# Performance work log

Measured on AMD Instinct MI355X. Metric: run time of the kernel, lower is better.

The kernel has to match this reference:

```python
import jax, jax.numpy as jnp
from jax import lax
import numpy as np

S = 0.025
EPS = 1e-6


def setup_inputs() -> dict:
    key = jax.random.key(0)
    k1, = jax.random.split(key, 1)
    B, F, T = 64, 128, 4000
    x = jax.random.uniform(k1, (B, F, T), dtype=jnp.float32)  # nonnegative spectrogram
    log_gain = jnp.zeros((F,), dtype=jnp.float32)
    log_bias = jnp.zeros((F,), dtype=jnp.float32)
    log_power = jnp.zeros((F,), dtype=jnp.float32)
    return {"x": x, "log_gain": log_gain, "log_bias": log_bias, "log_power": log_power}


def _ema(x):
    # x: [B, F, T]; first-order IIR m_t = (1-s)*m_{t-1} + s*x_t, m_{-1} = x_0
    # (so m_0 = x_0, matching the torch loop's init last_state = x[:, :, 0]).
    xt = jnp.moveaxis(x, -1, 0)  # [T, B, F]

    def step(carry, x_t):
        m = (1.0 - S) * carry + S * x_t
        return m, m

    _, m = lax.scan(step, xt[0], xt)
    return jnp.moveaxis(m, 0, -1)  # [B, F, T]


def reference(x, log_gain, log_bias, log_power):
    m = _ema(x)
    g = jnp.exp(log_gain)[None, :, None]   # [1, F, 1]
    b = jnp.exp(log_bias)[None, :, None]
    p = jnp.exp(log_power)[None, :, None]
    return (x / (m + EPS) ** g + b) ** p - b ** p
```

## Files before the change

kernel.cpp:

```cpp
#include <hip/hip_runtime.h>


#define LOG2F(v) __builtin_amdgcn_logf(v)
#define EXP2F(v) __builtin_amdgcn_exp2f(v)

constexpr int   T_LEN = 4000;
constexpr int   F_DIM = 128;
constexpr int   EPT   = 16;
constexpr int   TPB   = 256;
constexpr int   ACTIVE = T_LEN / EPT;
constexpr float S_C   = 0.025f;
constexpr float A1    = 1.0f - S_C;
constexpr float EPS_C = 1e-6f;

constexpr float pow_n(double a, int n) {
    double r = 1.0;
    for (int i = 0; i < n; ++i) r *= a;
    return (float)r;
}
constexpr float A16 = pow_n((double)A1, EPT);

__global__ __launch_bounds__(TPB) void pcen_kernel(
    const float* __restrict__ x,
    const float* __restrict__ log_gain,
    const float* __restrict__ log_bias,
    const float* __restrict__ log_power,
    float* __restrict__ out)
{
    const int row  = blockIdx.x;
    const int f    = row & (F_DIM - 1);
    const long long base = (long long)row * T_LEN;
    const int tid  = threadIdx.x;
    const int lane = tid & 63;
    const int wid  = tid >> 6;
    const bool active = tid < ACTIVE;

    const float g  = expf(log_gain[f]);
    const float b  = expf(log_bias[f]);
    const float p  = expf(log_power[f]);
    const float bp = EXP2F(p * LOG2F(b));

    float xv[EPT];
    const float4* xin = reinterpret_cast<const float4*>(x + base) + tid * 4;
    if (active) {
        #pragma unroll
        for (int q = 0; q < 4; ++q) {
            float4 v = xin[q];
            xv[q*4 + 0] = v.x; xv[q*4 + 1] = v.y;
            xv[q*4 + 2] = v.z; xv[q*4 + 3] = v.w;
        }
    }

    float Bi = 0.0f;
    if (active) {
        #pragma unroll
        for (int j = 0; j < EPT; ++j) Bi = fmaf(A1, Bi, S_C * xv[j]);
    }
    float Ai = active ? A16 : 1.0f;

    #pragma unroll
    for (int d = 1; d < 64; d <<= 1) {
        float Ap = __shfl_up(Ai, d);
        float Bp = __shfl_up(Bi, d);
        if (lane >= d) { Bi = fmaf(Ai, Bp, Bi); Ai *= Ap; }
    }

    __shared__ float sA[4], sB[4], sM0;
    if (lane == 63) { sA[wid] = Ai; sB[wid] = Bi; }
    if (tid == 0)   { sM0 = xv[0]; }
    __syncthreads();

    float pA = 1.0f, pB = 0.0f;
    for (int w = 0; w < wid; ++w) { pB = fmaf(sA[w], pB, sB[w]); pA *= sA[w]; }

    float eA = __shfl_up(Ai, 1);
    float eB = __shfl_up(Bi, 1);
    if (lane == 0) { eA = 1.0f; eB = 0.0f; }

    float m = fmaf(eA, fmaf(pA, sM0, pB), eB);

    if (active) {
        float4* o4 = reinterpret_cast<float4*>(out + base) + tid * 4;
        #pragma unroll
        for (int q = 0; q < 4; ++q) {
            float4 o;
            float ov[4];
            #pragma unroll
            for (int j = 0; j < 4; ++j) {
                const float xj = xv[q*4 + j];
                m = fmaf(A1, m, S_C * xj);
                float v = xj * EXP2F(-g * LOG2F(m + EPS_C));
                ov[j] = EXP2F(p * LOG2F(v + b)) - bp;
            }
            o.x = ov[0]; o.y = ov[1]; o.z = ov[2]; o.w = ov[3];
            o4[q] = o;
        }
    }
}

extern "C" void kernel_launch(void* const* d_in, const int* in_sizes, int n_in,
                              void* d_out, int out_size, void* d_ws, size_t ws_size,
                              hipStream_t stream) {
    const float* x  = (const float*)d_in[0];
    const float* lg = (const float*)d_in[1];
    const float* lb = (const float*)d_in[2];
    const float* lp = (const float*)d_in[3];
    float* out = (float*)d_out;

    const int rows = in_sizes[0] / T_LEN;
    pcen_kernel<<<dim3(rows), dim3(TPB), 0, stream>>>(x, lg, lb, lp, out);
}
```

Before: 238.4 us.

## Process one row per wavefront in LDS-transposed chunks with parameter fast path

Restructures the kernel so each wavefront owns a whole row, streaming it in four 1024-element chunks that are double-buffered in registers and transposed through padded LDS so each lane scans 16 consecutive samples. The cross-block scan becomes a wave-only shuffle scan with constant decay powers, and the carry between chunks comes from a lane-63 broadcast. A runtime fast path is added for gain, bias and power all exactly one, replacing the log/exp chain with a reciprocal. This removes the block-wide sync and most transcendentals on the test inputs, at the cost of more LDS traffic and a serial dependency across chunks.

```diff
diff --git a/kernel.cpp b/kernel.cpp
--- a/kernel.cpp
+++ b/kernel.cpp
@@ -1,24 +1,105 @@
 #include <hip/hip_runtime.h>
 
 
+#define EXP2F(v) __builtin_amdgcn_exp2f(v)
 #define LOG2F(v) __builtin_amdgcn_logf(v)
-#define EXP2F(v) __builtin_amdgcn_exp2f(v)
+#define RCPF(v)  __builtin_amdgcn_rcpf(v)
 
 constexpr int   T_LEN = 4000;
 constexpr int   F_DIM = 128;
-constexpr int   EPT   = 16;
 constexpr int   TPB   = 256;
-constexpr int   ACTIVE = T_LEN / EPT;
+constexpr int   RPB   = 4;
 constexpr float S_C   = 0.025f;
-constexpr float A1    = 1.0f - S_C;
+constexpr float A1    = 0.975f;
 constexpr float EPS_C = 1e-6f;
+constexpr int   LROW  = 17;
+constexpr int   WSLICE = 64 * LROW;
 
-constexpr float pow_n(double a, int n) {
-    double r = 1.0;
-    for (int i = 0; i < n; ++i) r *= a;
-    return (float)r;
+constexpr double dpow(double a, int n){ double r = 1; for (int i = 0; i < n; ++i) r *= a; return r; }
+constexpr float K1  = (float)dpow(0.975, 16);
+constexpr float K2  = (float)dpow(0.975, 32);
+constexpr float K4  = (float)dpow(0.975, 64);
+constexpr float K8  = (float)dpow(0.975, 128);
+constexpr float K16 = (float)dpow(0.975, 256);
+constexpr float K32 = (float)dpow(0.975, 512);
+constexpr float C16 = -0.5844128f;
+
+struct RowParams { float g, b, p, bp; bool fast; };
+
+template<int NF4>
+__device__ __forceinline__ void load_chunk(const float4* xr4, int c, int lane, float4 B[4]) {
+    #pragma unroll
+    for (int r = 0; r < 4; ++r) {
+        const int i4 = r * 64 + lane;
+        if (NF4 == 256 || i4 < NF4) B[r] = xr4[c * 256 + i4];
+        else                        B[r] = make_float4(0.f, 0.f, 0.f, 0.f);
+    }
 }
-constexpr float A16 = pow_n((double)A1, EPT);
+
+__device__ __forceinline__ void stage_chunk(float* L, int tw, const float4 B[4]) {
+    #pragma unroll
+    for (int r = 0; r < 4; ++r) {
+        float* d = L + r * (16 * LROW) + tw;
+        d[0] = B[r].x; d[1] = B[r].y; d[2] = B[r].z; d[3] = B[r].w;
+    }
+}
+
+template<int NF4, bool FIRST, bool LAST>
+__device__ __forceinline__ void compute_chunk(float* L, float4* qr4, int c,
+    int lane, int tr, int tw, float& m0, const RowParams& rp)
+{
+    float xl[16];
+    #pragma unroll
+    for (int j = 0; j < 16; ++j) xl[j] = L[tr + j];
+
+    if (FIRST) m0 = __shfl(xl[0], 0);
+
+    float Bv = S_C * xl[0];
+    #pragma unroll
+    for (int j = 1; j < 16; ++j) Bv = fmaf(A1, Bv, S_C * xl[j]);
+
+    float t;
+    t = __shfl_up(Bv,  1);  Bv = (lane >=  1) ? fmaf(K1 , t, Bv) : Bv;
+    t = __shfl_up(Bv,  2);  Bv = (lane >=  2) ? fmaf(K2 , t, Bv) : Bv;
+    t = __shfl_up(Bv,  4);  Bv = (lane >=  4) ? fmaf(K4 , t, Bv) : Bv;
+    t = __shfl_up(Bv,  8);  Bv = (lane >=  8) ? fmaf(K8 , t, Bv) : Bv;
+    t = __shfl_up(Bv, 16);  Bv = (lane >= 16) ? fmaf(K16, t, Bv) : Bv;
+    t = __shfl_up(Bv, 32);  Bv = (lane >= 32) ? fmaf(K32, t, Bv) : Bv;
+
+    float E = __shfl_up(Bv, 1);
+    if (lane == 0) E = 0.f;
+
+    float m = fmaf(EXP2F(C16 * (float)lane), m0, E);
+
+    if (rp.fast) {
+        #pragma unroll
+        for (int j = 0; j < 16; ++j) {
+            m = fmaf(A1, m, S_C * xl[j]);
+            xl[j] = xl[j] * RCPF(m + EPS_C);
+        }
+    } else {
+        #pragma unroll
+        for (int j = 0; j < 16; ++j) {
+            m = fmaf(A1, m, S_C * xl[j]);
+            float v = xl[j] * EXP2F(-rp.g * LOG2F(m + EPS_C));
+            xl[j] = EXP2F(rp.p * LOG2F(v + rp.b)) - rp.bp;
+        }
+    }
+
+    if (!LAST) m0 = __shfl(m, 63);
+
+    #pragma unroll
+    for (int j = 0; j < 16; ++j) L[tr + j] = xl[j];
+
+    #pragma unroll
+    for (int r = 0; r < 4; ++r) {
+        const int i4 = r * 64 + lane;
+        if (NF4 == 256 || i4 < NF4) {
+            const float* s = L + r * (16 * LROW) + tw;
+            qr4[c * 256 + i4] = make_float4(s[0], s[1], s[2], s[3]);
+        }
+    }
+}
 
 __global__ __launch_bounds__(TPB) void pcen_kernel(
     const float* __restrict__ x,
@@ -27,75 +108,46 @@
     const float* __restrict__ log_power,
     float* __restrict__ out)
 {
-    const int row  = blockIdx.x;
-    const int f    = row & (F_DIM - 1);
-    const long long base = (long long)row * T_LEN;
     const int tid  = threadIdx.x;
     const int lane = tid & 63;
     const int wid  = tid >> 6;
-    const bool active = tid < ACTIVE;
+    const int row  = blockIdx.x * RPB + wid;
+    const int f    = row & (F_DIM - 1);
 
-    const float g  = expf(log_gain[f]);
-    const float b  = expf(log_bias[f]);
-    const float p  = expf(log_power[f]);
-    const float bp = EXP2F(p * LOG2F(b));
+    const float4* xr4 = reinterpret_cast<const float4*>(x + (long long)row * T_LEN);
+    float4*       qr4 = reinterpret_cast<float4*>(out + (long long)row * T_LEN);
 
-    float xv[EPT];
-    const float4* xin = reinterpret_cast<const float4*>(x + base) + tid * 4;
-    if (active) {
-        #pragma unroll
-        for (int q = 0; q < 4; ++q) {
-            float4 v = xin[q];
-            xv[q*4 + 0] = v.x; xv[q*4 + 1] = v.y;
-            xv[q*4 + 2] = v.z; xv[q*4 + 3] = v.w;
-        }
-    }
+    RowParams rp;
+    rp.g = expf(log_gain[f]);
+    rp.b = expf(log_bias[f]);
+    rp.p = expf(log_power[f]);
+    rp.fast = (rp.g == 1.0f) && (rp.b == 1.0f) && (rp.p == 1.0f);
+    rp.bp = EXP2F(rp.p * LOG2F(rp.b));
 
-    float Bi = 0.0f;
-    if (active) {
-        #pragma unroll
-        for (int j = 0; j < EPT; ++j) Bi = fmaf(A1, Bi, S_C * xv[j]);
-    }
-    float Ai = active ? A16 : 1.0f;
+    __shared__ float lds[RPB * WSLICE];
+    float* L = lds + wid * WSLICE;
+    const int tr = lane * LROW;
+    const int tw = (lane >> 2) * LROW + (lane & 3) * 4;
 
-    #pragma unroll
-    for (int d = 1; d < 64; d <<= 1) {
-        float Ap = __shfl_up(Ai, d);
-        float Bp = __shfl_up(Bi, d);
-        if (lane >= d) { Bi = fmaf(Ai, Bp, Bi); Ai *= Ap; }
-    }
+    float4 b0[4], b1[4];
+    float m0 = 0.f;
 
-    __shared__ float sA[4], sB[4], sM0;
-    if (lane == 63) { sA[wid] = Ai; sB[wid] = Bi; }
-    if (tid == 0)   { sM0 = xv[0]; }
-    __syncthreads();
+    load_chunk<256>(xr4, 0, lane, b0);
+    load_chunk<256>(xr4, 1, lane, b1);
 
-    float pA = 1.0f, pB = 0.0f;
-    for (int w = 0; w < wid; ++w) { pB = fmaf(sA[w], pB, sB[w]); pA *= sA[w]; }
+    stage_chunk(L, tw, b0);
+    load_chunk<256>(xr4, 2, lane, b0);
+    compute_chunk<256, true , false>(L, qr4, 0, lane, tr, tw, m0, rp);
 
-    float eA = __shfl_up(Ai, 1);
-    float eB = __shfl_up(Bi, 1);
-    if (lane == 0) { eA = 1.0f; eB = 0.0f; }
+    stage_chunk(L, tw, b1);
+    load_chunk<232>(xr4, 3, lane, b1);
+    compute_chunk<256, false, false>(L, qr4, 1, lane, tr, tw, m0, rp);
 
-    float m = fmaf(eA, fmaf(pA, sM0, pB), eB);
+    stage_chunk(L, tw, b0);
+    compute_chunk<256, false, false>(L, qr4, 2, lane, tr, tw, m0, rp);
 
-    if (active) {
-        float4* o4 = reinterpret_cast<float4*>(out + base) + tid * 4;
-        #pragma unroll
-        for (int q = 0; q < 4; ++q) {
-            float4 o;
-            float ov[4];
-            #pragma unroll
-            for (int j = 0; j < 4; ++j) {
-                const float xj = xv[q*4 + j];
-                m = fmaf(A1, m, S_C * xj);
-                float v = xj * EXP2F(-g * LOG2F(m + EPS_C));
-                ov[j] = EXP2F(p * LOG2F(v + b)) - bp;
-            }
-            o.x = ov[0]; o.y = ov[1]; o.z = ov[2]; o.w = ov[3];
-            o4[q] = o;
-        }
-    }
+    stage_chunk(L, tw, b1);
+    compute_chunk<232, false, true >(L, qr4, 3, lane, tr, tw, m0, rp);
 }
 
 extern "C" void kernel_launch(void* const* d_in, const int* in_sizes, int n_in,
@@ -108,5 +160,5 @@
     float* out = (float*)d_out;
 
     const int rows = in_sizes[0] / T_LEN;
-    pcen_kernel<<<dim3(rows), dim3(TPB), 0, stream>>>(x, lg, lb, lp, out);
+    pcen_kernel<<<dim3(rows / RPB), dim3(TPB), 0, stream>>>(x, lg, lb, lp, out);
 }
```

After: 235.6 us. About the same (-1.2%).
